# Kernel tuning notes

Hardware: AMD Instinct MI355X
Metric: run time of the kernel (lower is better)

The kernel has to match this reference:

```python
import jax, jax.numpy as jnp
import numpy as np

B, H, W, C = 16, 64, 64, 256
NH = 8
KD = C // NH  # 32
SCALE = KD ** -0.5


def rotate_every_two(x):
    x1 = x[..., ::2]
    x2 = x[..., 1::2]
    return jnp.stack([-x2, x1], axis=-1).reshape(x.shape)


def theta_shift(x, sin, cos):
    return x * cos + rotate_every_two(x) * sin


def dwconv2d(x, w, b):
    # x: (b,h,w,c), w: (5,5,1,c) HWIO depthwise, pad 2
    y = jax.lax.conv_general_dilated(
        x, w, window_strides=(1, 1), padding=((2, 2), (2, 2)),
        dimension_numbers=("NHWC", "HWIO", "NHWC"), feature_group_count=x.shape[-1])
    return y + b


def setup_inputs() -> dict:
    key = jax.random.key(0)
    ks = jax.random.split(key, 12)
    s = 0.02
    return {
        "x": jax.random.normal(ks[0], (B, H, W, C), jnp.float32),
        "sin": jax.random.uniform(ks[1], (H, W, KD), jnp.float32, -1.0, 1.0),
        "cos": jax.random.uniform(ks[2], (H, W, KD), jnp.float32, -1.0, 1.0),
        "mask_h": jax.random.normal(ks[3], (NH, H, H), jnp.float32) * 0.1,
        "mask_w": jax.random.normal(ks[4], (NH, W, W), jnp.float32) * 0.1,
        "Wq": jax.random.normal(ks[5], (C, C), jnp.float32) * s,
        "bq": jnp.zeros((C,), jnp.float32),
        "Wk": jax.random.normal(ks[6], (C, C), jnp.float32) * s,
        "bk": jnp.zeros((C,), jnp.float32),
        "Wv": jax.random.normal(ks[7], (C, C), jnp.float32) * s,
        "bv": jnp.zeros((C,), jnp.float32),
        "conv_w": jax.random.normal(ks[8], (5, 5, 1, C), jnp.float32) * s,
        "conv_b": jnp.zeros((C,), jnp.float32),
        "Wo": jax.random.normal(ks[9], (C, C), jnp.float32) * s,
        "bo": jnp.zeros((C,), jnp.float32),
    }


def reference(x, sin, cos, mask_h, mask_w, Wq, bq, Wk, bk, Wv, bv, conv_w, conv_b, Wo, bo):
    b, h, w, _ = x.shape
    n = mask_w.shape[0]
    kd = sin.shape[-1]

    q = x @ Wq + bq
    k = (x @ Wk + bk) * SCALE
    v = x @ Wv + bv
    lepe = dwconv2d(v, conv_w, conv_b)

    # (b,n,h,w,d)
    q = q.reshape(b, h, w, n, kd).transpose(0, 3, 1, 2, 4)
    k = k.reshape(b, h, w, n, kd).transpose(0, 3, 1, 2, 4)
    qr = theta_shift(q, sin, cos)
    kr = theta_shift(k, sin, cos)

    # width attention: rows independent
    qk_w = jnp.einsum("bhnwd,bhnvd->bhnwv", qr.transpose(0, 2, 1, 3, 4), kr.transpose(0, 2, 1, 3, 4))
    qk_w = jax.nn.softmax(qk_w + mask_w, axis=-1)
    vv = v.reshape(b, h, w, n, -1).transpose(0, 1, 3, 2, 4)  # (b,h,n,w,d2)
    vv = jnp.einsum("bhnwv,bhnvd->bhnwd", qk_w, vv)

    # height attention: columns independent
    qr_h = qr.transpose(0, 3, 1, 2, 4)  # (b,w,n,h,d)
    kr_h = kr.transpose(0, 3, 1, 2, 4)
    vv = vv.transpose(0, 3, 2, 1, 4)  # (b,w,n,h,d2)
    qk_h = jnp.einsum("bwnhd,bwngd->bwnhg", qr_h, kr_h)
    qk_h = jax.nn.softmax(qk_h + mask_h, axis=-1)
    out = jnp.einsum("bwnhg,bwngd->bwnhd", qk_h, vv)

    out = out.transpose(0, 3, 1, 2, 4).reshape(b, h, w, -1)  # (b,h,w,n*d2)
    out = out + lepe
    return out @ Wo + bo
```

## Files before the change

### kernel.cpp

```cpp
#include <hip/hip_runtime.h>

typedef __attribute__((ext_vector_type(8))) short bf16x8;
typedef __attribute__((ext_vector_type(4))) float f32x4;

constexpr int B  = 16;
constexpr int H  = 64;
constexpr int W  = 64;
constexpr int C  = 256;
constexpr int NH = 8;
constexpr int KD = 32;
constexpr float SCALE = 0.17677669529663687f;
constexpr int M_TOT = B * H * W;
constexpr size_t NEL = (size_t)B * H * W * C;

__device__ __forceinline__ unsigned short f2bf(float f) {
    union { float f; unsigned int u; } x; x.f = f;
    unsigned int u = x.u;
    unsigned int r = (u + 0x7fffu + ((u >> 16) & 1u)) >> 16;
    return (unsigned short)r;
}
__device__ __forceinline__ float bf2f(unsigned short s) {
    union { unsigned int u; float f; } x; x.u = ((unsigned int)s) << 16; return x.f;
}
__device__ __forceinline__ float bf_lo(unsigned int u) {
    union { unsigned int u; float f; } x; x.u = u << 16; return x.f;
}
__device__ __forceinline__ float bf_hi(unsigned int u) {
    union { unsigned int u; float f; } x; x.u = u & 0xffff0000u; return x.f;
}
__device__ __forceinline__ unsigned int pack2(float a, float b) {
    return (unsigned int)f2bf(a) | ((unsigned int)f2bf(b) << 16);
}
__device__ __forceinline__ int swz(int row, int kp8) {
    return row * 32 + (kp8 ^ (((row >> 2) & 3) << 3));
}

__global__ __launch_bounds__(256) void prep_x16(const float* __restrict__ x,
                                                unsigned short* __restrict__ x16) {
    size_t i8 = ((size_t)blockIdx.x * 256 + threadIdx.x) * 8;
    float4 f0 = *(const float4*)(x + i8);
    float4 f1 = *(const float4*)(x + i8 + 4);
    uint4 o;
    o.x = pack2(f0.x, f0.y); o.y = pack2(f0.z, f0.w);
    o.z = pack2(f1.x, f1.y); o.w = pack2(f1.z, f1.w);
    *(uint4*)(x16 + i8) = o;
}

__global__ __launch_bounds__(256) void trans_w(const float* __restrict__ src,
                                               unsigned short* __restrict__ dst) {
    int tid = blockIdx.x * 256 + threadIdx.x;
    int n = tid >> 5, k0 = (tid & 31) << 3;
    unsigned int p[4];
#pragma unroll
    for (int j = 0; j < 4; ++j) {
        float a  = src[(size_t)(k0 + 2 * j) * 256 + n];
        float b2 = src[(size_t)(k0 + 2 * j + 1) * 256 + n];
        p[j] = pack2(a, b2);
    }
    uint4 o = {p[0], p[1], p[2], p[3]};
    *(uint4*)(dst + (size_t)n * 256 + k0) = o;
}

__global__ __launch_bounds__(256) void qkv_mfma(
    const unsigned short* __restrict__ x16, const unsigned short* __restrict__ Wt16,
    const float* __restrict__ bq, const float* __restrict__ bk, const float* __restrict__ bv,
    const float* __restrict__ sin_t, const float* __restrict__ cos_t,
    unsigned short* __restrict__ qr, unsigned short* __restrict__ kr,
    unsigned short* __restrict__ v16)
{
    __shared__ __align__(16) short As[128 * 32];
    __shared__ __align__(16) short Bs[128 * 32];

    const int t = threadIdx.x;
    const int lane = t & 63, wid = t >> 6;
    const int wr = wid >> 1, wc = wid & 1;
    const int m0 = blockIdx.x * 128;
    const int n0 = blockIdx.y * 128;
    const int matid = blockIdx.y >> 1;

    f32x4 acc[4][4];
#pragma unroll
    for (int i = 0; i < 4; ++i)
#pragma unroll
        for (int j = 0; j < 4; ++j)
#pragma unroll
            for (int q = 0; q < 4; ++q) acc[i][j][q] = 0.f;

    const int row_s = t >> 2;
    const int kp_s  = (t & 3) << 3;

    for (int ks = 0; ks < 8; ++ks) {
        const int k0 = ks * 32;
        const unsigned short* ap = x16 + (size_t)(m0 + row_s) * 256 + k0 + kp_s;
        uint4 a0 = *(const uint4*)ap;
        uint4 a1 = *(const uint4*)(ap + 64 * 256);
        const unsigned short* bp = Wt16 + (size_t)(n0 + row_s) * 256 + k0 + kp_s;
        uint4 b0 = *(const uint4*)bp;
        uint4 b1 = *(const uint4*)(bp + 64 * 256);

        __syncthreads();
        *(uint4*)(&As[swz(row_s,      kp_s)]) = a0;
        *(uint4*)(&As[swz(row_s + 64, kp_s)]) = a1;
        *(uint4*)(&Bs[swz(row_s,      kp_s)]) = b0;
        *(uint4*)(&Bs[swz(row_s + 64, kp_s)]) = b1;
        __syncthreads();

        bf16x8 af[4], bf[4];
        const int rsel = lane & 15, kg8 = (lane >> 4) << 3;
#pragma unroll
        for (int i = 0; i < 4; ++i)
            af[i] = *(const bf16x8*)(&As[swz(wr * 64 + i * 16 + rsel, kg8)]);
#pragma unroll
        for (int j = 0; j < 4; ++j)
            bf[j] = *(const bf16x8*)(&Bs[swz(wc * 64 + j * 16 + rsel, kg8)]);
#pragma unroll
        for (int i = 0; i < 4; ++i)
#pragma unroll
            for (int j = 0; j < 4; ++j)
                acc[i][j] = __builtin_amdgcn_mfma_f32_16x16x32_bf16(af[i], bf[j], acc[i][j], 0, 0, 0);
    }

    const int col_l = lane & 15, rowg = (lane >> 4) << 2;
    if (matid == 2) {
#pragma unroll
        for (int i = 0; i < 4; ++i)
#pragma unroll
            for (int j = 0; j < 4; ++j) {
                int nn = (n0 & 255) + wc * 64 + j * 16 + col_l;
                float bias = bv[nn];
#pragma unroll
                for (int r = 0; r < 4; ++r) {
                    int m = m0 + wr * 64 + i * 16 + rowg + r;
                    v16[(size_t)m * 256 + nn] = f2bf(acc[i][j][r] + bias);
                }
            }
    } else {
        const float sc = matid ? SCALE : 1.0f;
        const float* __restrict__ bias = matid ? bk : bq;
        unsigned short* __restrict__ dst = matid ? kr : qr;
        const int par = lane & 1;
#pragma unroll
        for (int i = 0; i < 4; ++i)
#pragma unroll
            for (int j = 0; j < 4; ++j) {
                int nn = (n0 & 255) + wc * 64 + j * 16 + col_l;
                int nh = nn >> 5, d = nn & 31;
                float bs = bias[nn];
#pragma unroll
                for (int r = 0; r < 4; ++r) {
                    int m = m0 + wr * 64 + i * 16 + rowg + r;
                    float val = (acc[i][j][r] + bs) * sc;
                    float p = __shfl_xor(val, 1);
                    int bb = m >> 12, hh = (m >> 6) & 63, ww = m & 63;
                    size_t ti = ((size_t)(hh << 6) + ww) * 32 + d;
                    float cs = cos_t[ti], sn = sin_t[ti];
                    float ov = par ? (val * cs + p * sn) : (val * cs - p * sn);
                    dst[((((size_t)bb * 8 + nh) * 64 + hh) * 64 + ww) * 32 + d] = f2bf(ov);
                }
            }
    }
}

__global__ __launch_bounds__(256) void conv_kernel(
    const unsigned short* __restrict__ v, const float* __restrict__ cw,
    const float* __restrict__ cb, unsigned short* __restrict__ lepe)
{
    size_t tid = (size_t)blockIdx.x * 256 + threadIdx.x;
    const int c8 = (int)(tid & 31) << 3;
    const int w  = (int)(tid >> 5) & 63;
    const int h  = (int)(tid >> 11) & 63;
    const int b  = (int)(tid >> 17);

    float acc[8];
    {
        float4 cb0 = *(const float4*)(cb + c8);
        float4 cb1 = *(const float4*)(cb + c8 + 4);
        acc[0] = cb0.x; acc[1] = cb0.y; acc[2] = cb0.z; acc[3] = cb0.w;
        acc[4] = cb1.x; acc[5] = cb1.y; acc[6] = cb1.z; acc[7] = cb1.w;
    }

    const unsigned short* __restrict__ vb = v + (size_t)b * 4096 * 256 + c8;
#pragma unroll
    for (int dy = 0; dy < 5; ++dy) {
        int yy = h + dy - 2;
        if (yy < 0 || yy >= 64) continue;
#pragma unroll
        for (int dx = 0; dx < 5; ++dx) {
            int xx = w + dx - 2;
            if (xx < 0 || xx >= 64) continue;
            uint4 rv = *(const uint4*)(vb + (size_t)(yy * 64 + xx) * 256);
            const float* wp = cw + (dy * 5 + dx) * 256 + c8;
            float4 w0 = *(const float4*)wp;
            float4 w1 = *(const float4*)(wp + 4);
            acc[0] += bf_lo(rv.x) * w0.x; acc[1] += bf_hi(rv.x) * w0.y;
            acc[2] += bf_lo(rv.y) * w0.z; acc[3] += bf_hi(rv.y) * w0.w;
            acc[4] += bf_lo(rv.z) * w1.x; acc[5] += bf_hi(rv.z) * w1.y;
            acc[6] += bf_lo(rv.w) * w1.z; acc[7] += bf_hi(rv.w) * w1.w;
        }
    }

    uint4 ov;
    ov.x = pack2(acc[0], acc[1]); ov.y = pack2(acc[2], acc[3]);
    ov.z = pack2(acc[4], acc[5]); ov.w = pack2(acc[6], acc[7]);
    *(uint4*)(lepe + tid * 8) = ov;
}

template <int AXIS>
__global__ __launch_bounds__(256) void attn_mfma(
    const unsigned short* __restrict__ qr, const unsigned short* __restrict__ kr,
    const unsigned short* __restrict__ vin, const float* __restrict__ mask,
    const unsigned short* __restrict__ addin, unsigned short* __restrict__ outp)
{
    __shared__ __align__(16) short qs[64 * 40];
    __shared__ __align__(16) short ks[64 * 40];
    __shared__ __align__(16) short vt[32 * 72];
    __shared__ __align__(16) short P [64 * 72];

    const int t    = threadIdx.x;
    const int lane = t & 63, wv = t >> 6;
    const int bid  = blockIdx.x;
    const int nh   = bid & 7;
    const int pos  = (bid >> 3) & 63;
    const int b    = bid >> 9;

    size_t qbase, vbase;
    int qstride, vstride;
    if (AXIS == 0) {
        qbase   = ((size_t)(b * 8 + nh) * 64 + pos) * 2048;
        qstride = 32;
        vbase   = ((size_t)(b * 64 + pos) * 64) * 256 + nh * 32;
        vstride = 256;
    } else {
        qbase   = ((size_t)(b * 8 + nh) * 64) * 2048 + pos * 32;
        qstride = 2048;
        vbase   = ((size_t)b * 64 * 64) * 256 + pos * 256 + nh * 32;
        vstride = 16384;
    }

    {
        int row = t >> 2, c8 = (t & 3) << 3;
        uint4 rq = *(const uint4*)(qr + qbase + (size_t)row * qstride + c8);
        *(uint4*)(&qs[row * 40 + c8]) = rq;
        uint4 rk = *(const uint4*)(kr + qbase + (size_t)row * qstride + c8);
        *(uint4*)(&ks[row * 40 + c8]) = rk;
        uint4 rv = *(const uint4*)(vin + vbase + (size_t)row * vstride + c8);
        const unsigned short* pv = (const unsigned short*)&rv;
#pragma unroll
        for (int j = 0; j < 8; ++j) vt[(c8 + j) * 72 + row] = pv[j];
    }
    __syncthreads();

    const int rsel = lane & 15;
    const int kg   = (lane >> 4) << 3;
    const int rowg = (lane >> 4) << 2;

    bf16x8 aq = *(const bf16x8*)(&qs[(wv * 16 + rsel) * 40 + kg]);
    f32x4 s[4];
#pragma unroll
    for (int j = 0; j < 4; ++j) {
        f32x4 z = {0.f, 0.f, 0.f, 0.f};
        bf16x8 bk8 = *(const bf16x8*)(&ks[(j * 16 + rsel) * 40 + kg]);
        s[j] = __builtin_amdgcn_mfma_f32_16x16x32_bf16(aq, bk8, z, 0, 0, 0);
    }

    const float* __restrict__ mrow = mask + (size_t)nh * 4096;
#pragma unroll
    for (int r = 0; r < 4; ++r) {
        const int grow = wv * 16 + rowg + r;
#pragma unroll
        for (int j = 0; j < 4; ++j)
            s[j][r] += mrow[grow * 64 + j * 16 + rsel];
        float mx = fmaxf(fmaxf(s[0][r], s[1][r]), fmaxf(s[2][r], s[3][r]));
        mx = fmaxf(mx, __shfl_xor(mx, 1));
        mx = fmaxf(mx, __shfl_xor(mx, 2));
        mx = fmaxf(mx, __shfl_xor(mx, 4));
        mx = fmaxf(mx, __shfl_xor(mx, 8));
        float e0 = __expf(s[0][r] - mx), e1 = __expf(s[1][r] - mx);
        float e2 = __expf(s[2][r] - mx), e3 = __expf(s[3][r] - mx);
        float sum = e0 + e1 + e2 + e3;
        sum += __shfl_xor(sum, 1);
        sum += __shfl_xor(sum, 2);
        sum += __shfl_xor(sum, 4);
        sum += __shfl_xor(sum, 8);
        float inv = 1.0f / sum;
        P[grow * 72 +      rsel] = f2bf(e0 * inv);
        P[grow * 72 + 16 + rsel] = f2bf(e1 * inv);
        P[grow * 72 + 32 + rsel] = f2bf(e2 * inv);
        P[grow * 72 + 48 + rsel] = f2bf(e3 * inv);
    }
    __syncthreads();

    f32x4 o[2];
#pragma unroll
    for (int n = 0; n < 2; ++n)
#pragma unroll
        for (int q = 0; q < 4; ++q) o[n][q] = 0.f;
#pragma unroll
    for (int kk = 0; kk < 2; ++kk) {
        bf16x8 ap = *(const bf16x8*)(&P[(wv * 16 + rsel) * 72 + kk * 32 + kg]);
#pragma unroll
        for (int n = 0; n < 2; ++n) {
            bf16x8 bv8 = *(const bf16x8*)(&vt[(n * 16 + rsel) * 72 + kk * 32 + kg]);
            o[n] = __builtin_amdgcn_mfma_f32_16x16x32_bf16(ap, bv8, o[n], 0, 0, 0);
        }
    }

#pragma unroll
    for (int n = 0; n < 2; ++n)
#pragma unroll
        for (int r = 0; r < 4; ++r) {
            const int grow = wv * 16 + rowg + r;
            size_t oidx = vbase + (size_t)grow * vstride + n * 16 + rsel;
            float val = o[n][r];
            if (AXIS == 1) val += bf2f(addin[oidx]);
            outp[oidx] = f2bf(val);
        }
}

__global__ __launch_bounds__(256) void gemm_out_mfma(
    const unsigned short* __restrict__ y16, const unsigned short* __restrict__ Wot16,
    const float* __restrict__ bo, float* __restrict__ out)
{
    __shared__ __align__(16) short As[128 * 32];
    __shared__ __align__(16) short Bs[128 * 32];

    const int t = threadIdx.x;
    const int lane = t & 63, wid = t >> 6;
    const int wr = wid >> 1, wc = wid & 1;
    const int m0 = blockIdx.x * 128;
    const int n0 = blockIdx.y * 128;

    f32x4 acc[4][4];
#pragma unroll
    for (int i = 0; i < 4; ++i)
#pragma unroll
        for (int j = 0; j < 4; ++j)
#pragma unroll
            for (int q = 0; q < 4; ++q) acc[i][j][q] = 0.f;

    const int row_s = t >> 2;
    const int kp_s  = (t & 3) << 3;

    for (int ks = 0; ks < 8; ++ks) {
        const int k0 = ks * 32;
        const unsigned short* ap = y16 + (size_t)(m0 + row_s) * 256 + k0 + kp_s;
        uint4 a0 = *(const uint4*)ap;
        uint4 a1 = *(const uint4*)(ap + 64 * 256);
        const unsigned short* bp = Wot16 + (size_t)(n0 + row_s) * 256 + k0 + kp_s;
        uint4 b0 = *(const uint4*)bp;
        uint4 b1 = *(const uint4*)(bp + 64 * 256);

        __syncthreads();
        *(uint4*)(&As[swz(row_s,      kp_s)]) = a0;
        *(uint4*)(&As[swz(row_s + 64, kp_s)]) = a1;
        *(uint4*)(&Bs[swz(row_s,      kp_s)]) = b0;
        *(uint4*)(&Bs[swz(row_s + 64, kp_s)]) = b1;
        __syncthreads();

        bf16x8 af[4], bf[4];
        const int rsel = lane & 15, kg8 = (lane >> 4) << 3;
#pragma unroll
        for (int i = 0; i < 4; ++i)
            af[i] = *(const bf16x8*)(&As[swz(wr * 64 + i * 16 + rsel, kg8)]);
#pragma unroll
        for (int j = 0; j < 4; ++j)
            bf[j] = *(const bf16x8*)(&Bs[swz(wc * 64 + j * 16 + rsel, kg8)]);
#pragma unroll
        for (int i = 0; i < 4; ++i)
#pragma unroll
            for (int j = 0; j < 4; ++j)
                acc[i][j] = __builtin_amdgcn_mfma_f32_16x16x32_bf16(af[i], bf[j], acc[i][j], 0, 0, 0);
    }

    const int col_l = lane & 15, rowg = (lane >> 4) << 2;
#pragma unroll
    for (int i = 0; i < 4; ++i)
#pragma unroll
        for (int j = 0; j < 4; ++j) {
            int nn = n0 + wc * 64 + j * 16 + col_l;
            float bias = bo[nn];
#pragma unroll
            for (int r = 0; r < 4; ++r) {
                int m = m0 + wr * 64 + i * 16 + rowg + r;
                out[(size_t)m * 256 + nn] = acc[i][j][r] + bias;
            }
        }
}

extern "C" void kernel_launch(void* const* d_in, const int* in_sizes, int n_in,
                              void* d_out, int out_size, void* d_ws, size_t ws_size,
                              hipStream_t stream) {
    const float* x      = (const float*)d_in[0];
    const float* sin_t  = (const float*)d_in[1];
    const float* cos_t  = (const float*)d_in[2];
    const float* mask_h = (const float*)d_in[3];
    const float* mask_w = (const float*)d_in[4];
    const float* Wq     = (const float*)d_in[5];
    const float* bq     = (const float*)d_in[6];
    const float* Wk     = (const float*)d_in[7];
    const float* bk     = (const float*)d_in[8];
    const float* Wv     = (const float*)d_in[9];
    const float* bv     = (const float*)d_in[10];
    const float* conv_w = (const float*)d_in[11];
    const float* conv_b = (const float*)d_in[12];
    const float* Wo     = (const float*)d_in[13];
    const float* bo     = (const float*)d_in[14];

    unsigned short* ws    = (unsigned short*)d_ws;
    unsigned short* v16   = ws;
    unsigned short* lepe16= v16 + NEL;
    unsigned short* qr16  = lepe16 + NEL;
    unsigned short* kr16  = qr16 + NEL;
    unsigned short* y16   = kr16 + NEL;
    unsigned short* Wt16  = y16 + NEL;
    unsigned short* Wot16 = Wt16 + 768 * 256;

    unsigned short* vv16 = (unsigned short*)d_out;
    unsigned short* x16  = (unsigned short*)d_out + NEL;

    prep_x16<<<(int)(NEL / 2048), 256, 0, stream>>>(x, x16);
    trans_w<<<32, 256, 0, stream>>>(Wq, Wt16);
    trans_w<<<32, 256, 0, stream>>>(Wk, Wt16 + 256 * 256);
    trans_w<<<32, 256, 0, stream>>>(Wv, Wt16 + 512 * 256);
    trans_w<<<32, 256, 0, stream>>>(Wo, Wot16);

    qkv_mfma<<<dim3(M_TOT / 128, 6), 256, 0, stream>>>(
        x16, Wt16, bq, bk, bv, sin_t, cos_t, qr16, kr16, v16);

    conv_kernel<<<(int)(NEL / 2048), 256, 0, stream>>>(v16, conv_w, conv_b, lepe16);

    attn_mfma<0><<<B * H * NH, 256, 0, stream>>>(qr16, kr16, v16, mask_w, nullptr, vv16);

    attn_mfma<1><<<B * W * NH, 256, 0, stream>>>(qr16, kr16, vv16, mask_h, lepe16, y16);

    gemm_out_mfma<<<dim3(M_TOT / 128, 2), 256, 0, stream>>>(y16, Wot16, bo, (float*)d_out);
}
```

Measured before the change: 260.6 us.

## Load GEMM tiles directly to LDS and vectorize QK rotary epilogue

The QKV and output GEMMs now stage their A and B tiles with global_load_lds, writing straight into the swizzled shared-memory layout instead of going through registers. The QKV kernel is split into a Q/K instance and a V instance. The Q/K instance swaps the MFMA operand order so each lane holds four consecutive channels of one pixel. That lets the rotary shift use in-register pairs and vectorized float4 sin/cos/bias loads with ushort4 stores, where before it needed a shuffle plus scalar loads and 2-byte stores. This adds an extra kernel launch, and the direct-to-LDS path depends on the lane address mapping matching the swizzle exactly.

```diff
diff --git a/kernel.cpp b/kernel.cpp
--- a/kernel.cpp
+++ b/kernel.cpp
@@ -35,6 +35,12 @@
     return row * 32 + (kp8 ^ (((row >> 2) & 3) << 3));
 }
 
+typedef const __attribute__((address_space(1))) unsigned int gas_uint;
+typedef __attribute__((address_space(3))) unsigned int las_uint;
+__device__ __forceinline__ void gl16(const unsigned short* g, unsigned short* l) {
+    __builtin_amdgcn_global_load_lds((gas_uint*)g, (las_uint*)l, 16, 0, 0);
+}
+
 __global__ __launch_bounds__(256) void prep_x16(const float* __restrict__ x,
                                                 unsigned short* __restrict__ x16) {
     size_t i8 = ((size_t)blockIdx.x * 256 + threadIdx.x) * 8;
@@ -61,22 +67,25 @@
     *(uint4*)(dst + (size_t)n * 256 + k0) = o;
 }
 
-__global__ __launch_bounds__(256) void qkv_mfma(
+template <int QK>
+__global__ __launch_bounds__(256) void qkv_part(
     const unsigned short* __restrict__ x16, const unsigned short* __restrict__ Wt16,
     const float* __restrict__ bq, const float* __restrict__ bk, const float* __restrict__ bv,
     const float* __restrict__ sin_t, const float* __restrict__ cos_t,
     unsigned short* __restrict__ qr, unsigned short* __restrict__ kr,
     unsigned short* __restrict__ v16)
 {
-    __shared__ __align__(16) short As[128 * 32];
-    __shared__ __align__(16) short Bs[128 * 32];
+    __shared__ __align__(16) unsigned short As[128 * 32];
+    __shared__ __align__(16) unsigned short Bs[128 * 32];
 
     const int t = threadIdx.x;
     const int lane = t & 63, wid = t >> 6;
     const int wr = wid >> 1, wc = wid & 1;
     const int m0 = blockIdx.x * 128;
-    const int n0 = blockIdx.y * 128;
-    const int matid = blockIdx.y >> 1;
+    const int yb = blockIdx.y;
+    const int wrow0 = QK ? yb * 128 : 512 + yb * 128;
+    const int nb    = QK ? (yb & 1) * 128 : yb * 128;
+    const int matid = QK ? (yb >> 1) : 2;
 
     f32x4 acc[4][4];
 #pragma unroll
@@ -86,27 +95,27 @@
 #pragma unroll
             for (int q = 0; q < 4; ++q) acc[i][j][q] = 0.f;
 
-    const int row_s = t >> 2;
-    const int kp_s  = (t & 3) << 3;
+    const int lco = ((lane >> 2) << 8) + (((lane & 3) ^ (lane >> 4)) << 3);
+    const unsigned short* ag = x16 + (size_t)m0 * 256 + lco;
+    const unsigned short* bg = Wt16 + (size_t)wrow0 * 256 + lco;
+    unsigned short* al0 = As + wid * 16 * 32;
+    unsigned short* al1 = As + (64 + wid * 16) * 32;
+    unsigned short* bl0 = Bs + wid * 16 * 32;
+    unsigned short* bl1 = Bs + (64 + wid * 16) * 32;
+    const int rg0 = wid * 16 * 256, rg1 = (64 + wid * 16) * 256;
+
+    const int rsel = lane & 15, kg8 = (lane >> 4) << 3;
 
     for (int ks = 0; ks < 8; ++ks) {
         const int k0 = ks * 32;
-        const unsigned short* ap = x16 + (size_t)(m0 + row_s) * 256 + k0 + kp_s;
-        uint4 a0 = *(const uint4*)ap;
-        uint4 a1 = *(const uint4*)(ap + 64 * 256);
-        const unsigned short* bp = Wt16 + (size_t)(n0 + row_s) * 256 + k0 + kp_s;
-        uint4 b0 = *(const uint4*)bp;
-        uint4 b1 = *(const uint4*)(bp + 64 * 256);
-
         __syncthreads();
-        *(uint4*)(&As[swz(row_s,      kp_s)]) = a0;
-        *(uint4*)(&As[swz(row_s + 64, kp_s)]) = a1;
-        *(uint4*)(&Bs[swz(row_s,      kp_s)]) = b0;
-        *(uint4*)(&Bs[swz(row_s + 64, kp_s)]) = b1;
+        gl16(ag + rg0 + k0, al0);
+        gl16(ag + rg1 + k0, al1);
+        gl16(bg + rg0 + k0, bl0);
+        gl16(bg + rg1 + k0, bl1);
         __syncthreads();
 
         bf16x8 af[4], bf[4];
-        const int rsel = lane & 15, kg8 = (lane >> 4) << 3;
 #pragma unroll
         for (int i = 0; i < 4; ++i)
             af[i] = *(const bf16x8*)(&As[swz(wr * 64 + i * 16 + rsel, kg8)]);
@@ -116,17 +125,21 @@
 #pragma unroll
         for (int i = 0; i < 4; ++i)
 #pragma unroll
-            for (int j = 0; j < 4; ++j)
-                acc[i][j] = __builtin_amdgcn_mfma_f32_16x16x32_bf16(af[i], bf[j], acc[i][j], 0, 0, 0);
+            for (int j = 0; j < 4; ++j) {
+                if (QK)
+                    acc[i][j] = __builtin_amdgcn_mfma_f32_16x16x32_bf16(bf[j], af[i], acc[i][j], 0, 0, 0);
+                else
+                    acc[i][j] = __builtin_amdgcn_mfma_f32_16x16x32_bf16(af[i], bf[j], acc[i][j], 0, 0, 0);
+            }
     }
 
     const int col_l = lane & 15, rowg = (lane >> 4) << 2;
-    if (matid == 2) {
+    if (QK == 0) {
 #pragma unroll
         for (int i = 0; i < 4; ++i)
 #pragma unroll
             for (int j = 0; j < 4; ++j) {
-                int nn = (n0 & 255) + wc * 64 + j * 16 + col_l;
+                int nn = nb + wc * 64 + j * 16 + col_l;
                 float bias = bv[nn];
 #pragma unroll
                 for (int r = 0; r < 4; ++r) {
@@ -138,26 +151,30 @@
         const float sc = matid ? SCALE : 1.0f;
         const float* __restrict__ bias = matid ? bk : bq;
         unsigned short* __restrict__ dst = matid ? kr : qr;
-        const int par = lane & 1;
-#pragma unroll
-        for (int i = 0; i < 4; ++i)
+#pragma unroll
+        for (int i = 0; i < 4; ++i) {
+            const int m = m0 + wr * 64 + i * 16 + col_l;
+            const int bb = m >> 12, hh = (m >> 6) & 63, ww = m & 63;
+            const size_t pixbase = ((size_t)hh * 64 + ww) * 32;
 #pragma unroll
             for (int j = 0; j < 4; ++j) {
-                int nn = (n0 & 255) + wc * 64 + j * 16 + col_l;
-                int nh = nn >> 5, d = nn & 31;
-                float bs = bias[nn];
-#pragma unroll
-                for (int r = 0; r < 4; ++r) {
-                    int m = m0 + wr * 64 + i * 16 + rowg + r;
-                    float val = (acc[i][j][r] + bs) * sc;
-                    float p = __shfl_xor(val, 1);
-                    int bb = m >> 12, hh = (m >> 6) & 63, ww = m & 63;
-                    size_t ti = ((size_t)(hh << 6) + ww) * 32 + d;
-                    float cs = cos_t[ti], sn = sin_t[ti];
-                    float ov = par ? (val * cs + p * sn) : (val * cs - p * sn);
-                    dst[((((size_t)bb * 8 + nh) * 64 + hh) * 64 + ww) * 32 + d] = f2bf(ov);
-                }
+                const int n = nb + wc * 64 + j * 16 + rowg;
+                const int nh = n >> 5, db = n & 31;
+                float4 bias4 = *(const float4*)(bias + n);
+                float4 cs4 = *(const float4*)(cos_t + pixbase + db);
+                float4 sn4 = *(const float4*)(sin_t + pixbase + db);
+                float v0 = (acc[i][j][0] + bias4.x) * sc;
+                float v1 = (acc[i][j][1] + bias4.y) * sc;
+                float v2 = (acc[i][j][2] + bias4.z) * sc;
+                float v3 = (acc[i][j][3] + bias4.w) * sc;
+                ushort4 o;
+                o.x = f2bf(v0 * cs4.x - v1 * sn4.x);
+                o.y = f2bf(v1 * cs4.y + v0 * sn4.y);
+                o.z = f2bf(v2 * cs4.z - v3 * sn4.z);
+                o.w = f2bf(v3 * cs4.w + v2 * sn4.w);
+                *(ushort4*)(dst + ((((size_t)bb * 8 + nh) * 64 + hh) * 64 + ww) * 32 + db) = o;
             }
+        }
     }
 }
 
@@ -321,8 +338,8 @@
     const unsigned short* __restrict__ y16, const unsigned short* __restrict__ Wot16,
     const float* __restrict__ bo, float* __restrict__ out)
 {
-    __shared__ __align__(16) short As[128 * 32];
-    __shared__ __align__(16) short Bs[128 * 32];
+    __shared__ __align__(16) unsigned short As[128 * 32];
+    __shared__ __align__(16) unsigned short Bs[128 * 32];
 
     const int t = threadIdx.x;
     const int lane = t & 63, wid = t >> 6;
@@ -338,27 +355,27 @@
 #pragma unroll
             for (int q = 0; q < 4; ++q) acc[i][j][q] = 0.f;
 
-    const int row_s = t >> 2;
-    const int kp_s  = (t & 3) << 3;
+    const int lco = ((lane >> 2) << 8) + (((lane & 3) ^ (lane >> 4)) << 3);
+    const unsigned short* ag = y16 + (size_t)m0 * 256 + lco;
+    const unsigned short* bg = Wot16 + (size_t)n0 * 256 + lco;
+    unsigned short* al0 = As + wid * 16 * 32;
+    unsigned short* al1 = As + (64 + wid * 16) * 32;
+    unsigned short* bl0 = Bs + wid * 16 * 32;
+    unsigned short* bl1 = Bs + (64 + wid * 16) * 32;
+    const int rg0 = wid * 16 * 256, rg1 = (64 + wid * 16) * 256;
+
+    const int rsel = lane & 15, kg8 = (lane >> 4) << 3;
 
     for (int ks = 0; ks < 8; ++ks) {
         const int k0 = ks * 32;
-        const unsigned short* ap = y16 + (size_t)(m0 + row_s) * 256 + k0 + kp_s;
-        uint4 a0 = *(const uint4*)ap;
-        uint4 a1 = *(const uint4*)(ap + 64 * 256);
-        const unsigned short* bp = Wot16 + (size_t)(n0 + row_s) * 256 + k0 + kp_s;
-        uint4 b0 = *(const uint4*)bp;
-        uint4 b1 = *(const uint4*)(bp + 64 * 256);
-
         __syncthreads();
-        *(uint4*)(&As[swz(row_s,      kp_s)]) = a0;
-        *(uint4*)(&As[swz(row_s + 64, kp_s)]) = a1;
-        *(uint4*)(&Bs[swz(row_s,      kp_s)]) = b0;
-        *(uint4*)(&Bs[swz(row_s + 64, kp_s)]) = b1;
+        gl16(ag + rg0 + k0, al0);
+        gl16(ag + rg1 + k0, al1);
+        gl16(bg + rg0 + k0, bl0);
+        gl16(bg + rg1 + k0, bl1);
         __syncthreads();
 
         bf16x8 af[4], bf[4];
-        const int rsel = lane & 15, kg8 = (lane >> 4) << 3;
 #pragma unroll
         for (int i = 0; i < 4; ++i)
             af[i] = *(const bf16x8*)(&As[swz(wr * 64 + i * 16 + rsel, kg8)]);
@@ -424,8 +441,10 @@
     trans_w<<<32, 256, 0, stream>>>(Wv, Wt16 + 512 * 256);
     trans_w<<<32, 256, 0, stream>>>(Wo, Wot16);
 
-    qkv_mfma<<<dim3(M_TOT / 128, 6), 256, 0, stream>>>(
+    qkv_part<1><<<dim3(M_TOT / 128, 4), 256, 0, stream>>>(
         x16, Wt16, bq, bk, bv, sin_t, cos_t, qr16, kr16, v16);
+    qkv_part<0><<<dim3(M_TOT / 128, 2), 256, 0, stream>>>(
+        x16, Wt16, bq, bk, bv, sin_t, cos_t, qr16, kr16, v16);
 
     conv_kernel<<<(int)(NEL / 2048), 256, 0, stream>>>(v16, conv_w, conv_b, lepe16);
 
```

Measured after the change: 275.0 us. 1.06x slower.

## Vectorize QKV epilogue stores via swapped MFMA operands and tile conv over four pixels

Applied to the files above, without the earlier changes.

The QKV GEMM now passes the MFMA operands in swapped order, so each lane holds four consecutive output channels for one pixel. That lets the epilogue read bias, sin and cos as float4, do the rotary pairing inside the lane with no shuffle, and write 8-byte vector stores in place of scattered 2-byte stores. The depthwise conv now has each thread compute four adjacent output pixels from a shared 8-pixel row window, which cuts redundant loads of v and of the weights, at the cost of more registers per thread. The launch grid is reduced to match.

```diff
diff --git a/kernel.cpp b/kernel.cpp
--- a/kernel.cpp
+++ b/kernel.cpp
@@ -31,6 +31,10 @@
 __device__ __forceinline__ unsigned int pack2(float a, float b) {
     return (unsigned int)f2bf(a) | ((unsigned int)f2bf(b) << 16);
 }
+__device__ __forceinline__ void cvt8(uint4 rv, float* f) {
+    f[0] = bf_lo(rv.x); f[1] = bf_hi(rv.x); f[2] = bf_lo(rv.y); f[3] = bf_hi(rv.y);
+    f[4] = bf_lo(rv.z); f[5] = bf_hi(rv.z); f[6] = bf_lo(rv.w); f[7] = bf_hi(rv.w);
+}
 __device__ __forceinline__ int swz(int row, int kp8) {
     return row * 32 + (kp8 ^ (((row >> 2) & 3) << 3));
 }
@@ -68,8 +72,8 @@
     unsigned short* __restrict__ qr, unsigned short* __restrict__ kr,
     unsigned short* __restrict__ v16)
 {
-    __shared__ __align__(16) short As[128 * 32];
-    __shared__ __align__(16) short Bs[128 * 32];
+    __shared__ __align__(16) unsigned short As[128 * 32];
+    __shared__ __align__(16) unsigned short Bs[128 * 32];
 
     const int t = threadIdx.x;
     const int lane = t & 63, wid = t >> 6;
@@ -77,6 +81,7 @@
     const int m0 = blockIdx.x * 128;
     const int n0 = blockIdx.y * 128;
     const int matid = blockIdx.y >> 1;
+    const int nb = n0 & 255;
 
     f32x4 acc[4][4];
 #pragma unroll
@@ -117,47 +122,54 @@
         for (int i = 0; i < 4; ++i)
 #pragma unroll
             for (int j = 0; j < 4; ++j)
-                acc[i][j] = __builtin_amdgcn_mfma_f32_16x16x32_bf16(af[i], bf[j], acc[i][j], 0, 0, 0);
+                acc[i][j] = __builtin_amdgcn_mfma_f32_16x16x32_bf16(bf[j], af[i], acc[i][j], 0, 0, 0);
     }
 
     const int col_l = lane & 15, rowg = (lane >> 4) << 2;
     if (matid == 2) {
 #pragma unroll
-        for (int i = 0; i < 4; ++i)
+        for (int i = 0; i < 4; ++i) {
+            const int m = m0 + wr * 64 + i * 16 + col_l;
 #pragma unroll
             for (int j = 0; j < 4; ++j) {
-                int nn = (n0 & 255) + wc * 64 + j * 16 + col_l;
-                float bias = bv[nn];
-#pragma unroll
-                for (int r = 0; r < 4; ++r) {
-                    int m = m0 + wr * 64 + i * 16 + rowg + r;
-                    v16[(size_t)m * 256 + nn] = f2bf(acc[i][j][r] + bias);
-                }
+                const int nn = nb + wc * 64 + j * 16 + rowg;
+                float4 bias4 = *(const float4*)(bv + nn);
+                ushort4 o;
+                o.x = f2bf(acc[i][j][0] + bias4.x);
+                o.y = f2bf(acc[i][j][1] + bias4.y);
+                o.z = f2bf(acc[i][j][2] + bias4.z);
+                o.w = f2bf(acc[i][j][3] + bias4.w);
+                *(ushort4*)(v16 + (size_t)m * 256 + nn) = o;
             }
+        }
     } else {
         const float sc = matid ? SCALE : 1.0f;
         const float* __restrict__ bias = matid ? bk : bq;
         unsigned short* __restrict__ dst = matid ? kr : qr;
-        const int par = lane & 1;
-#pragma unroll
-        for (int i = 0; i < 4; ++i)
+#pragma unroll
+        for (int i = 0; i < 4; ++i) {
+            const int m = m0 + wr * 64 + i * 16 + col_l;
+            const int bb = m >> 12, hh = (m >> 6) & 63, ww = m & 63;
+            const size_t pixbase = ((size_t)hh * 64 + ww) * 32;
 #pragma unroll
             for (int j = 0; j < 4; ++j) {
-                int nn = (n0 & 255) + wc * 64 + j * 16 + col_l;
-                int nh = nn >> 5, d = nn & 31;
-                float bs = bias[nn];
-#pragma unroll
-                for (int r = 0; r < 4; ++r) {
-                    int m = m0 + wr * 64 + i * 16 + rowg + r;
-                    float val = (acc[i][j][r] + bs) * sc;
-                    float p = __shfl_xor(val, 1);
-                    int bb = m >> 12, hh = (m >> 6) & 63, ww = m & 63;
-                    size_t ti = ((size_t)(hh << 6) + ww) * 32 + d;
-                    float cs = cos_t[ti], sn = sin_t[ti];
-                    float ov = par ? (val * cs + p * sn) : (val * cs - p * sn);
-                    dst[((((size_t)bb * 8 + nh) * 64 + hh) * 64 + ww) * 32 + d] = f2bf(ov);
-                }
+                const int n = nb + wc * 64 + j * 16 + rowg;
+                const int nh = n >> 5, db = n & 31;
+                float4 bias4 = *(const float4*)(bias + n);
+                float4 cs4 = *(const float4*)(cos_t + pixbase + db);
+                float4 sn4 = *(const float4*)(sin_t + pixbase + db);
+                float v0 = (acc[i][j][0] + bias4.x) * sc;
+                float v1 = (acc[i][j][1] + bias4.y) * sc;
+                float v2 = (acc[i][j][2] + bias4.z) * sc;
+                float v3 = (acc[i][j][3] + bias4.w) * sc;
+                ushort4 o;
+                o.x = f2bf(v0 * cs4.x - v1 * sn4.x);
+                o.y = f2bf(v1 * cs4.y + v0 * sn4.y);
+                o.z = f2bf(v2 * cs4.z - v3 * sn4.z);
+                o.w = f2bf(v3 * cs4.w + v2 * sn4.w);
+                *(ushort4*)(dst + ((((size_t)bb * 8 + nh) * 64 + hh) * 64 + ww) * 32 + db) = o;
             }
+        }
     }
 }
 
@@ -167,42 +179,62 @@
 {
     size_t tid = (size_t)blockIdx.x * 256 + threadIdx.x;
     const int c8 = (int)(tid & 31) << 3;
-    const int w  = (int)(tid >> 5) & 63;
-    const int h  = (int)(tid >> 11) & 63;
-    const int b  = (int)(tid >> 17);
-
-    float acc[8];
+    const int w0 = ((int)(tid >> 5) & 15) << 2;
+    const int h  = (int)(tid >> 9) & 63;
+    const int b  = (int)(tid >> 15);
+
+    float acc[4][8];
     {
         float4 cb0 = *(const float4*)(cb + c8);
         float4 cb1 = *(const float4*)(cb + c8 + 4);
-        acc[0] = cb0.x; acc[1] = cb0.y; acc[2] = cb0.z; acc[3] = cb0.w;
-        acc[4] = cb1.x; acc[5] = cb1.y; acc[6] = cb1.z; acc[7] = cb1.w;
+#pragma unroll
+        for (int o = 0; o < 4; ++o) {
+            acc[o][0] = cb0.x; acc[o][1] = cb0.y; acc[o][2] = cb0.z; acc[o][3] = cb0.w;
+            acc[o][4] = cb1.x; acc[o][5] = cb1.y; acc[o][6] = cb1.z; acc[o][7] = cb1.w;
+        }
     }
 
     const unsigned short* __restrict__ vb = v + (size_t)b * 4096 * 256 + c8;
 #pragma unroll
     for (int dy = 0; dy < 5; ++dy) {
-        int yy = h + dy - 2;
+        const int yy = h + dy - 2;
         if (yy < 0 || yy >= 64) continue;
+        float rowf[8][8];
+#pragma unroll
+        for (int j = 0; j < 8; ++j) {
+            const int xx = w0 + j - 2;
+            if (xx < 0 || xx >= 64) {
+#pragma unroll
+                for (int q = 0; q < 8; ++q) rowf[j][q] = 0.f;
+            } else {
+                uint4 rv = *(const uint4*)(vb + (size_t)(yy * 64 + xx) * 256);
+                cvt8(rv, rowf[j]);
+            }
+        }
 #pragma unroll
         for (int dx = 0; dx < 5; ++dx) {
-            int xx = w + dx - 2;
-            if (xx < 0 || xx >= 64) continue;
-            uint4 rv = *(const uint4*)(vb + (size_t)(yy * 64 + xx) * 256);
             const float* wp = cw + (dy * 5 + dx) * 256 + c8;
-            float4 w0 = *(const float4*)wp;
-            float4 w1 = *(const float4*)(wp + 4);
-            acc[0] += bf_lo(rv.x) * w0.x; acc[1] += bf_hi(rv.x) * w0.y;
-            acc[2] += bf_lo(rv.y) * w0.z; acc[3] += bf_hi(rv.y) * w0.w;
-            acc[4] += bf_lo(rv.z) * w1.x; acc[5] += bf_hi(rv.z) * w1.y;
-            acc[6] += bf_lo(rv.w) * w1.z; acc[7] += bf_hi(rv.w) * w1.w;
-        }
-    }
-
-    uint4 ov;
-    ov.x = pack2(acc[0], acc[1]); ov.y = pack2(acc[2], acc[3]);
-    ov.z = pack2(acc[4], acc[5]); ov.w = pack2(acc[6], acc[7]);
-    *(uint4*)(lepe + tid * 8) = ov;
+            float4 wv0 = *(const float4*)wp;
+            float4 wv1 = *(const float4*)(wp + 4);
+#pragma unroll
+            for (int o = 0; o < 4; ++o) {
+                const float* rf = rowf[dx + o];
+                acc[o][0] += rf[0] * wv0.x; acc[o][1] += rf[1] * wv0.y;
+                acc[o][2] += rf[2] * wv0.z; acc[o][3] += rf[3] * wv0.w;
+                acc[o][4] += rf[4] * wv1.x; acc[o][5] += rf[5] * wv1.y;
+                acc[o][6] += rf[6] * wv1.z; acc[o][7] += rf[7] * wv1.w;
+            }
+        }
+    }
+
+    unsigned short* __restrict__ op = lepe + (((size_t)(b * 64 + h) * 64) + w0) * 256 + c8;
+#pragma unroll
+    for (int o = 0; o < 4; ++o) {
+        uint4 ov;
+        ov.x = pack2(acc[o][0], acc[o][1]); ov.y = pack2(acc[o][2], acc[o][3]);
+        ov.z = pack2(acc[o][4], acc[o][5]); ov.w = pack2(acc[o][6], acc[o][7]);
+        *(uint4*)(op + (size_t)o * 256) = ov;
+    }
 }
 
 template <int AXIS>
@@ -321,8 +353,8 @@
     const unsigned short* __restrict__ y16, const unsigned short* __restrict__ Wot16,
     const float* __restrict__ bo, float* __restrict__ out)
 {
-    __shared__ __align__(16) short As[128 * 32];
-    __shared__ __align__(16) short Bs[128 * 32];
+    __shared__ __align__(16) unsigned short As[128 * 32];
+    __shared__ __align__(16) unsigned short Bs[128 * 32];
 
     const int t = threadIdx.x;
     const int lane = t & 63, wid = t >> 6;
@@ -427,7 +459,7 @@
     qkv_mfma<<<dim3(M_TOT / 128, 6), 256, 0, stream>>>(
         x16, Wt16, bq, bk, bv, sin_t, cos_t, qr16, kr16, v16);
 
-    conv_kernel<<<(int)(NEL / 2048), 256, 0, stream>>>(v16, conv_w, conv_b, lepe16);
+    conv_kernel<<<(int)(NEL / 32 / 256), 256, 0, stream>>>(v16, conv_w, conv_b, lepe16);
 
     attn_mfma<0><<<B * H * NH, 256, 0, stream>>>(qr16, kr16, v16, mask_w, nullptr, vv16);
 
```

Result: faster. 248.3 us (-4.7%).
